# Optimization experiments

Hardware: AMD Instinct MI355X
Metric: run time of the kernel (lower is better)

The kernel has to match this reference:

```python
import jax, jax.numpy as jnp
import numpy as np

B, S, D = 2, 1024, 1024
H, HD = 16, 64
E_R = 31          # routed experts (n_experts - n_shared)
K_ACT = 3         # activated routed experts (n_activated - n_shared)
INTER = 1024      # expert inter dim = int(D*4*0.25)
EPS = 1e-5
BASE = 10000.0


def setup_inputs() -> dict:
    key = jax.random.key(0)
    ks = jax.random.split(key, 24)
    s = 0.02
    theta = (BASE ** (-jnp.arange(HD // 2, dtype=jnp.float32) * 2.0 / HD))
    inp = {
        'x': jax.random.normal(ks[0], (B, S, D), jnp.float32),
        'positions': jnp.arange(S, dtype=jnp.int32),
        'theta': theta,
        'gamma1': jnp.ones((D,), jnp.float32),
        'gamma2': jnp.ones((D,), jnp.float32),
        'q_w': jax.random.normal(ks[1], (D, H * HD), jnp.float32) * s,
        'q_b': jnp.zeros((H * HD,), jnp.float32),
        'k_w': jax.random.normal(ks[2], (D, H * HD), jnp.float32) * s,
        'k_b': jnp.zeros((H * HD,), jnp.float32),
        'v_w': jax.random.normal(ks[3], (D, H * HD), jnp.float32) * s,
        'v_b': jnp.zeros((H * HD,), jnp.float32),
        'o_w': jax.random.normal(ks[4], (H * HD, D), jnp.float32) * s,
        'o_b': jnp.zeros((D,), jnp.float32),
        'router_w': jax.random.normal(ks[5], (D, E_R), jnp.float32) * s,
        'router_b': jnp.zeros((E_R,), jnp.float32),
        'sh_w1': jax.random.normal(ks[6], (D, INTER), jnp.float32) * s,
        'sh_b1': jnp.zeros((INTER,), jnp.float32),
        'sh_w2': jax.random.normal(ks[7], (INTER, D), jnp.float32) * s,
        'sh_b2': jnp.zeros((D,), jnp.float32),
        're_w1': jax.random.normal(ks[8], (E_R, D, INTER), jnp.float32) * s,
        're_b1': jnp.zeros((E_R, INTER), jnp.float32),
        're_w2': jax.random.normal(ks[9], (E_R, INTER, D), jnp.float32) * s,
        're_b2': jnp.zeros((E_R, D), jnp.float32),
    }
    return inp


def _rmsnorm(x, gamma):
    rms = jnp.sqrt(jnp.mean(x * x, axis=-1, keepdims=True) + EPS)
    return x / rms * gamma


def _rope(x, theta):
    # x: [B,H,S,HD]; split even/odd, rotate, concat halves (matches source)
    seq = x.shape[2]
    angles = jnp.arange(seq, dtype=theta.dtype)[:, None] * theta  # [S, HD/2]
    cos = jnp.cos(angles)[None, None]
    sin = jnp.sin(angles)[None, None]
    x1, x2 = x[..., 0::2], x[..., 1::2]
    return jnp.concatenate([x1 * cos - x2 * sin, x1 * sin + x2 * cos], axis=-1)


def _forward(x, theta, gamma1, gamma2, q_w, q_b, k_w, k_b, v_w, v_b, o_w, o_b,
             router_w, router_b, sh_w1, sh_b1, sh_w2, sh_b2,
             re_w1, re_b1, re_w2, re_b2):
    b, s, d = x.shape
    xn = _rmsnorm(x, gamma1)
    # --- MHA ---
    q = (xn @ q_w + q_b).reshape(b, s, H, HD).transpose(0, 2, 1, 3)
    k = (xn @ k_w + k_b).reshape(b, s, H, HD).transpose(0, 2, 1, 3)
    v = (xn @ v_w + v_b).reshape(b, s, H, HD).transpose(0, 2, 1, 3)
    q = _rope(q, theta)
    k = _rope(k, theta)
    scale = 1.0 / np.sqrt(HD)
    scores = jnp.einsum('bhqd,bhkd->bhqk', q, k) * scale
    causal = jnp.tril(jnp.ones((s, s), dtype=bool))
    scores = jnp.where(causal, scores, -jnp.inf)
    attn = jax.nn.softmax(scores, axis=-1)
    ctx = jnp.einsum('bhqk,bhkd->bhqd', attn, v)
    ctx = ctx.transpose(0, 2, 1, 3).reshape(b, s, H * HD)
    attn_out = ctx @ o_w + o_b + xn
    # --- MoE ---
    an = _rmsnorm(attn_out, gamma2)
    shared = jax.nn.gelu(an @ sh_w1 + sh_b1, approximate=False) @ sh_w2 + sh_b2
    logits = an @ router_w + router_b                      # [B,S,E]
    aff = jax.nn.softmax(logits, axis=-1)
    topv, topi = jax.lax.top_k(aff, K_ACT)                 # [B,S,K]
    gates = jnp.sum(jax.nn.one_hot(topi, E_R, dtype=aff.dtype) * topv[..., None], axis=-2)  # [B,S,E]
    h = jax.nn.gelu(jnp.einsum('bsd,edh->besh', an, re_w1) + re_b1[None, :, None, :],
                    approximate=False)                     # [B,E,S,INTER]
    routed = jnp.einsum('bse,besh,ehd->bsd', gates, h, re_w2) \
           + jnp.einsum('bse,ed->bsd', gates, re_b2)
    return shared + routed + an + attn_out


def reference(x, positions, theta, gamma1, gamma2, q_w, q_b, k_w, k_b, v_w, v_b,
              o_w, o_b, router_w, router_b, sh_w1, sh_b1, sh_w2, sh_b2,
              re_w1, re_b1, re_w2, re_b2):
    del positions  # unused by the original forward (RoPE builds its own arange)
    return _forward(x, theta, gamma1, gamma2, q_w, q_b, k_w, k_b, v_w, v_b,
                    o_w, o_b, router_w, router_b, sh_w1, sh_b1, sh_w2, sh_b2,
                    re_w1, re_b1, re_w2, re_b2)
```

## Files before the change

kernel.cpp:

```cpp
#include <hip/hip_runtime.h>
#include <math.h>

typedef unsigned short u16;
typedef short s8v __attribute__((ext_vector_type(8)));
typedef u16 u4v __attribute__((ext_vector_type(4)));
typedef float f4v __attribute__((ext_vector_type(4)));

#define MFMA16(a,b,c) __builtin_amdgcn_mfma_f32_16x16x32_bf16((a),(b),(c),0,0,0)
#define GLDS16(g, l) __builtin_amdgcn_global_load_lds( \
    (const __attribute__((address_space(1))) unsigned int*)(g), \
    (__attribute__((address_space(3))) unsigned int*)(l), 16, 0, 0)

#define N_TOK 2048
#define SEQ   1024

__device__ __forceinline__ u16 f2b(float f){
  union { float f; unsigned u; } v; v.f = f;
  return (u16)((v.u + 0x7FFFu + ((v.u >> 16) & 1u)) >> 16);
}
__device__ __forceinline__ float b2f(u16 b){
  union { unsigned u; float f; } v; v.u = ((unsigned)b) << 16; return v.f;
}
__device__ __forceinline__ float gelu_f(float x){
  return 0.5f*x*(1.0f + erff(x*0.70710678118654752f));
}

__global__ __launch_bounds__(256) void rmsnorm_k(const float* __restrict__ x,
    const float* __restrict__ gamma, float* __restrict__ outf, u16* __restrict__ outb)
{
  const int t = blockIdx.x, tid = threadIdx.x;
  const float* xr = x + (size_t)t * 1024;
  float4 xv = *(const float4*)(xr + tid*4);
  float ss = xv.x*xv.x + xv.y*xv.y + xv.z*xv.z + xv.w*xv.w;
  #pragma unroll
  for (int off = 32; off; off >>= 1) ss += __shfl_down(ss, off);
  __shared__ float red[4];
  if ((tid & 63) == 0) red[tid >> 6] = ss;
  __syncthreads();
  float inv = rsqrtf((red[0]+red[1]+red[2]+red[3]) * (1.0f/1024.0f) + 1e-5f);
  float4 gv = *(const float4*)(gamma + tid*4);
  float4 o;
  o.x = xv.x*inv*gv.x; o.y = xv.y*inv*gv.y; o.z = xv.z*inv*gv.z; o.w = xv.w*inv*gv.w;
  *(float4*)(outf + (size_t)t*1024 + tid*4) = o;
  u4v ob = { f2b(o.x), f2b(o.y), f2b(o.z), f2b(o.w) };
  *(u4v*)(outb + (size_t)t*1024 + tid*4) = ob;
}

__device__ __forceinline__ void transT_body(const float* __restrict__ W, u16* __restrict__ Wt)
{
  __shared__ __align__(16) u16 T[64][68];
  const int tid = threadIdx.x;
  const int k0 = blockIdx.x*64, n0 = blockIdx.y*64;
  #pragma unroll
  for (int j = 0; j < 4; j++) {
    int q = j*256 + tid; int r = q >> 4, c4 = q & 15;
    float4 v = *(const float4*)(W + (size_t)(k0 + r)*1024 + n0 + c4*4);
    T[c4*4+0][r] = f2b(v.x); T[c4*4+1][r] = f2b(v.y);
    T[c4*4+2][r] = f2b(v.z); T[c4*4+3][r] = f2b(v.w);
  }
  __syncthreads();
  #pragma unroll
  for (int j = 0; j < 4; j++) {
    int q = j*256 + tid; int n = q >> 4, c4 = q & 15;
    u4v o = *(const u4v*)&T[n][c4*4];
    *(u4v*)(Wt + (size_t)(n0 + n)*1024 + k0 + c4*4) = o;
  }
}

__global__ __launch_bounds__(256) void transT6_k(
    const float* s0, const float* s1, const float* s2,
    const float* s3, const float* s4, const float* s5,
    u16* d0, u16* d1, u16* d2, u16* d3, u16* d4, u16* d5)
{
  const float* S; u16* D;
  switch (blockIdx.z) {
    case 0: S=s0; D=d0; break; case 1: S=s1; D=d1; break;
    case 2: S=s2; D=d2; break; case 3: S=s3; D=d3; break;
    case 4: S=s4; D=d4; break; default: S=s5; D=d5; break;
  }
  transT_body(S, D);
}

__global__ __launch_bounds__(256) void transv_k(const u16* __restrict__ vb, u16* __restrict__ vt)
{
  __shared__ __align__(16) u16 T[64][72];
  const int tid = threadIdx.x;
  const int s0 = blockIdx.x*64, bh = blockIdx.y, b = bh>>4, h = bh&15;
  #pragma unroll
  for (int j = 0; j < 16; j++) {
    int q = j*256 + tid; int r = q >> 6, c = q & 63;
    T[c][r] = vb[(size_t)(b*SEQ + s0 + r)*1024 + h*64 + c];
  }
  __syncthreads();
  #pragma unroll
  for (int i = 0; i < 2; i++) {
    int q = tid*2 + i; int rr = q >> 3, c8 = q & 7;
    *(s8v*)(vt + (size_t)(bh*64 + rr)*1024 + s0 + c8*8) = *(const s8v*)&T[rr][c8*8];
  }
}

template<int MODE, int BM, int BN>
__global__ __launch_bounds__(256) void mmk(
    const u16* __restrict__ A,
    const u16* __restrict__ Wt0, const u16* __restrict__ Wt1, const u16* __restrict__ Wt2,
    const float* __restrict__ bias0, const float* __restrict__ bias1, const float* __restrict__ bias2,
    float* __restrict__ outf, u16* __restrict__ outb0, u16* __restrict__ outb1, u16* __restrict__ outb2,
    const float* __restrict__ add1, const float* __restrict__ add2,
    const int* __restrict__ gidx, const float* __restrict__ gatel,
    const int* __restrict__ counts, const int* __restrict__ offs,
    const int* __restrict__ wl, const int* __restrict__ ntl,
    const float* __restrict__ theta, const float* __restrict__ wf)
{
  constexpr bool EW = (MODE == 5 || MODE == 6);
  constexpr int MF = BM/32, NF = BN/32;
  constexpr int CA = BM/32, CB = BN/32;
  constexpr int BST = EW ? 72 : 64;
  __shared__ __align__(16) u16 As[BM*64];
  __shared__ __align__(16) u16 Bs[BN*BST];
  __shared__ int toks[(MODE==5) ? BM : 1];
  __shared__ float gts[(MODE==6) ? BM : 1];

  const int tid = threadIdx.x;
  const int wave = tid >> 6, lane = tid & 63, quad = lane >> 4, l15 = lane & 15;
  int row0 = blockIdx.y * BM;
  int col0 = blockIdx.x * BN;
  const u16* Wt = Wt0;
  const float* bias = bias0;
  const u16* Ab = A;
  const float* Wf = wf;
  int wsel = 0, e = 0, cnt = 0, off_e = 0;

  if (MODE == 7) {
    wsel = blockIdx.x >> 3;
    col0 = (blockIdx.x & 7) * BN;
    Wt   = (wsel == 0) ? Wt0 : ((wsel == 1) ? Wt1 : Wt2);
    bias = (wsel == 0) ? bias0 : ((wsel == 1) ? bias1 : bias2);
  }
  if (EW) {
    if ((int)blockIdx.y >= ntl[0]) return;
    const int w = wl[blockIdx.y];
    e = w >> 8;
    row0 = (w & 255) * BM;
    cnt = counts[e];
    Wf = wf + (size_t)e * 1024 * 1024;
    bias = bias0 + e * 1024;
    off_e = offs[e];
    if (MODE == 6) Ab = A + (size_t)off_e * 1024;
    if (tid < BM) {
      int ok = (row0 + tid) < cnt;
      if (MODE == 5) toks[tid] = ok ? gidx[e * N_TOK + row0 + tid] : 0;
      if (MODE == 6) gts[tid]  = ok ? gatel[e * N_TOK + row0 + tid] : 0.f;
    }
    __syncthreads();
  }

  const int lr8 = lane >> 3;
  const int lk  = (lane & 7) * 8;
  const u16* aptr[CA];
  const u16* bptr[CB];
  #pragma unroll
  for (int c = 0; c < CA; c++) {
    const int ar = wave*(BM/4) + c*8 + lr8;
    long garow;
    if (MODE == 5) {
      garow = toks[ar];
    } else if (MODE == 6) {
      int rr = row0 + ar; if (rr >= cnt) rr = cnt - 1; garow = rr;
    } else {
      garow = row0 + ar;
    }
    aptr[c] = Ab + (size_t)garow * 1024 + lk;
  }
  if (!EW) {
    #pragma unroll
    for (int c = 0; c < CB; c++) {
      const int br = wave*(BN/4) + c*8 + lr8;
      bptr[c] = Wt + (size_t)(col0 + br) * 1024 + lk;
    }
  }

  const int ewn  = tid & 127;
  const int kg0  = (tid >> 7) * 4;
  const float* ewp = EW ? (Wf + (size_t)(kg0*8)*1024 + col0 + ewn) : nullptr;

  f4v acc[MF][NF];
  #pragma unroll
  for (int i = 0; i < MF; i++)
    #pragma unroll
    for (int j = 0; j < NF; j++)
      acc[i][j] = (f4v){0.f,0.f,0.f,0.f};

  const int wr = (wave >> 1) * (BM/2), wc = (wave & 1) * (BN/2);

  for (int k0 = 0; k0 < 1024; k0 += 64) {
    float fb[EW ? 4 : 1][EW ? 8 : 1];
    if (EW) {
      const float* wp = ewp + (size_t)k0 * 1024;
      #pragma unroll
      for (int it = 0; it < 4; it++)
        #pragma unroll
        for (int i = 0; i < 8; i++)
          fb[it][i] = wp[(size_t)(it*8 + i)*1024];
    }
    __syncthreads();
    #pragma unroll
    for (int c = 0; c < CA; c++) GLDS16(aptr[c] + k0, As + (wave*(BM/4) + c*8)*64);
    if (EW) {
      #pragma unroll
      for (int it = 0; it < 4; it++) {
        s8v h;
        #pragma unroll
        for (int i = 0; i < 8; i++) h[i] = (short)f2b(fb[it][i]);
        *(s8v*)&Bs[ewn*BST + (kg0 + it)*8] = h;
      }
    } else {
      #pragma unroll
      for (int c = 0; c < CB; c++) GLDS16(bptr[c] + k0, Bs + (wave*(BN/4) + c*8)*64);
    }
    __syncthreads();
    s8v af[2][MF], bfr[2][NF];
    #pragma unroll
    for (int ks = 0; ks < 2; ks++) {
      #pragma unroll
      for (int mt = 0; mt < MF; mt++) af[ks][mt]  = *(const s8v*)&As[(wr + mt*16 + l15)*64 + ks*32 + quad*8];
      #pragma unroll
      for (int nt = 0; nt < NF; nt++) bfr[ks][nt] = *(const s8v*)&Bs[(wc + nt*16 + l15)*BST + ks*32 + quad*8];
    }
    #pragma unroll
    for (int ks = 0; ks < 2; ks++)
      #pragma unroll
      for (int mt = 0; mt < MF; mt++)
        #pragma unroll
        for (int nt = 0; nt < NF; nt++)
          acc[mt][nt] = MFMA16(af[ks][mt], bfr[ks][nt], acc[mt][nt]);
  }

  #pragma unroll
  for (int mt = 0; mt < MF; mt++) {
    #pragma unroll
    for (int reg = 0; reg < 4; reg++) {
      const int lr = wr + mt*16 + quad*4 + reg;
      const size_t gr = row0 + lr;
      #pragma unroll
      for (int nt = 0; nt < NF; nt++) {
        const int n = wc + nt*16 + l15 + col0;
        float v = acc[mt][nt][reg] + bias[n];
        if (MODE == 7) {
          if (wsel == 2) {
            outb2[gr*1024 + n] = f2b(v);
          } else {
            float pv = __shfl_xor(v, 1);
            const int hd = n & 63;
            const int j = hd >> 1;
            const int s = (int)(gr & (SEQ - 1));
            float ang = (float)s * theta[j];
            float sn, cs;
            sincosf(ang, &sn, &cs);
            float res; int col;
            if (hd & 1) { res = pv*sn + v*cs; col = (n & ~63) | (32 + j); }
            else        { res = v*cs - pv*sn; col = (n & ~63) | j; }
            u16 bv = f2b(res);
            if (wsel == 0) outb0[gr*1024 + col] = bv;
            else           outb1[gr*1024 + col] = bv;
          }
        } else if (MODE == 3) {
          outf[gr*1024 + n] = v + add1[gr*1024 + n];
        } else if (MODE == 2) {
          outb0[gr*1024 + n] = f2b(gelu_f(v));
        } else if (MODE == 4) {
          outf[gr*1024 + n] = v + add1[gr*1024 + n] + add2[gr*1024 + n];
        } else if (MODE == 5) {
          if (row0 + lr < cnt)
            outb0[(size_t)(off_e + row0 + lr)*1024 + n] = f2b(gelu_f(v));
        } else if (MODE == 6) {
          if (row0 + lr < cnt)
            outf[(size_t)(off_e + row0 + lr)*1024 + n] = gts[lr] * v;
        }
      }
    }
  }
}

__global__ __launch_bounds__(256) void attn_k(const u16* __restrict__ qg,
    const u16* __restrict__ kg, const u16* __restrict__ vtg, u16* __restrict__ ctx)
{
  const int qt = (blockIdx.y < 16) ? blockIdx.x : (15 - blockIdx.x);
  const int bh = blockIdx.y, b = bh >> 4, h = bh & 15;
  const int tid = threadIdx.x, wave = tid >> 6, lane = tid & 63;
  const int quad = lane >> 4, l15 = lane & 15;
  __shared__ __align__(16) u16 Ks[64][72];
  __shared__ __align__(16) u16 Vt[64][72];
  __shared__ __align__(16) u16 Ps[4][16][72];

  s8v aq0, aq1;
  {
    const size_t qrow = (size_t)(b*SEQ + qt*64 + wave*16 + l15);
    aq0 = *(const s8v*)(qg + qrow*1024 + h*64 + quad*8);
    aq1 = *(const s8v*)(qg + qrow*1024 + h*64 + 32 + quad*8);
  }
  f4v oac[4];
  #pragma unroll
  for (int i = 0; i < 4; i++) oac[i] = (f4v){0.f,0.f,0.f,0.f};
  float mi[4] = {-INFINITY,-INFINITY,-INFINITY,-INFINITY};
  float li[4] = {0.f,0.f,0.f,0.f};

  for (int kt = 0; kt <= qt; kt++) {
    __syncthreads();
    #pragma unroll
    for (int ii = 0; ii < 2; ii++) {
      int c = tid*2 + ii, r = c >> 3, c8 = c & 7;
      *(s8v*)&Ks[r][c8*8] = *(const s8v*)(kg + (size_t)(b*SEQ + kt*64 + r)*1024 + h*64 + c8*8);
      *(s8v*)&Vt[r][c8*8] = *(const s8v*)(vtg + (size_t)(bh*64 + r)*1024 + kt*64 + c8*8);
    }
    __syncthreads();

    f4v s[4];
    #pragma unroll
    for (int nt = 0; nt < 4; nt++) {
      f4v z = (f4v){0.f,0.f,0.f,0.f};
      s8v bk0 = *(const s8v*)&Ks[nt*16 + l15][quad*8];
      s8v bk1 = *(const s8v*)&Ks[nt*16 + l15][32 + quad*8];
      z = MFMA16(aq0, bk0, z);
      z = MFMA16(aq1, bk1, z);
      s[nt] = z;
    }
    float sc[4][4];
    const int rowl = wave*16 + quad*4;
    #pragma unroll
    for (int nt = 0; nt < 4; nt++) {
      #pragma unroll
      for (int r = 0; r < 4; r++) {
        float v = s[nt][r] * 0.125f;
        if (kt == qt && (nt*16 + l15) > (rowl + r)) v = -INFINITY;
        sc[nt][r] = v;
      }
    }
    float alpha[4];
    #pragma unroll
    for (int r = 0; r < 4; r++) {
      float v0 = fmaxf(fmaxf(sc[0][r], sc[1][r]), fmaxf(sc[2][r], sc[3][r]));
      v0 = fmaxf(v0, __shfl_xor(v0, 1));
      v0 = fmaxf(v0, __shfl_xor(v0, 2));
      v0 = fmaxf(v0, __shfl_xor(v0, 4));
      v0 = fmaxf(v0, __shfl_xor(v0, 8));
      float mnew = fmaxf(mi[r], v0);
      alpha[r] = __expf(mi[r] - mnew);
      mi[r] = mnew;
    }
    float psum[4] = {0.f,0.f,0.f,0.f};
    #pragma unroll
    for (int nt = 0; nt < 4; nt++) {
      #pragma unroll
      for (int r = 0; r < 4; r++) {
        float p = __expf(sc[nt][r] - mi[r]);
        psum[r] += p;
        Ps[wave][quad*4 + r][nt*16 + l15] = f2b(p);
      }
    }
    #pragma unroll
    for (int r = 0; r < 4; r++) {
      float ps = psum[r];
      ps += __shfl_xor(ps, 1);
      ps += __shfl_xor(ps, 2);
      ps += __shfl_xor(ps, 4);
      ps += __shfl_xor(ps, 8);
      li[r] = li[r]*alpha[r] + ps;
    }
    #pragma unroll
    for (int ht = 0; ht < 4; ht++) {
      f4v o = oac[ht];
      o[0] *= alpha[0]; o[1] *= alpha[1]; o[2] *= alpha[2]; o[3] *= alpha[3];
      oac[ht] = o;
    }
    asm volatile("s_waitcnt lgkmcnt(0)" ::: "memory");
    s8v pf0 = *(const s8v*)&Ps[wave][l15][quad*8];
    s8v pf1 = *(const s8v*)&Ps[wave][l15][32 + quad*8];
    #pragma unroll
    for (int ht = 0; ht < 4; ht++) {
      s8v vf0 = *(const s8v*)&Vt[ht*16 + l15][quad*8];
      s8v vf1 = *(const s8v*)&Vt[ht*16 + l15][32 + quad*8];
      oac[ht] = MFMA16(pf0, vf0, oac[ht]);
      oac[ht] = MFMA16(pf1, vf1, oac[ht]);
    }
  }
  float inv[4];
  #pragma unroll
  for (int r = 0; r < 4; r++) inv[r] = 1.f / li[r];
  #pragma unroll
  for (int ht = 0; ht < 4; ht++) {
    #pragma unroll
    for (int r = 0; r < 4; r++) {
      size_t row = (size_t)(b*SEQ + qt*64 + wave*16 + quad*4 + r);
      ctx[row*1024 + h*64 + ht*16 + l15] = f2b(oac[ht][r] * inv[r]);
    }
  }
}

__global__ __launch_bounds__(256) void router_k(const float* __restrict__ an,
    const float* __restrict__ rw, const float* __restrict__ rb,
    int* __restrict__ counts, int* __restrict__ tok_list, float* __restrict__ gate_list,
    int* __restrict__ tok_e, int* __restrict__ tok_s)
{
  const int t = blockIdx.x, tid = threadIdx.x;
  const int e = tid & 31, ch = tid >> 5;
  float part = 0.f;
  if (e < 31) {
    const float* ar = an + (size_t)t*1024 + ch*128;
    const float* wp = rw + (size_t)(ch*128)*31 + e;
    #pragma unroll 8
    for (int d = 0; d < 128; d++) part += ar[d] * wp[d*31];
  }
  __shared__ float red[8][32];
  __shared__ float lgs[32];
  red[ch][e] = part;
  __syncthreads();
  if (tid < 31) {
    float s = 0.f;
    #pragma unroll
    for (int c = 0; c < 8; c++) s += red[c][tid];
    lgs[tid] = s + rb[tid];
  }
  __syncthreads();
  if (tid == 0) {
    float m = -1e30f;
    for (int i = 0; i < 31; i++) m = fmaxf(m, lgs[i]);
    float den = 0.f;
    for (int i = 0; i < 31; i++) den += __expf(lgs[i] - m);
    float invd = 1.f/den;
    unsigned used = 0;
    for (int kk = 0; kk < 3; kk++) {
      int best = 0; float bv = -3e30f;
      for (int i = 0; i < 31; i++) if (!((used>>i)&1u) && lgs[i] > bv) { bv = lgs[i]; best = i; }
      used |= (1u << best);
      float gate = __expf(lgs[best] - m) * invd;
      int slot = atomicAdd(&counts[best], 1);
      tok_list[best*N_TOK + slot] = t;
      gate_list[best*N_TOK + slot] = gate;
      tok_e[t*3 + kk] = best;
      tok_s[t*3 + kk] = slot;
    }
  }
}

__global__ void scan_k(const int* __restrict__ counts, int* __restrict__ offs,
                       int* __restrict__ wl, int* __restrict__ ntl){
  if (threadIdx.x == 0) {
    int s = 0, nt = 0;
    for (int i = 0; i < 31; i++){
      offs[i] = s; s += counts[i];
      int t = (counts[i] + 63) >> 6;
      for (int r = 0; r < t; r++) wl[nt++] = (i << 8) | r;
    }
    ntl[0] = nt;
  }
}

__global__ __launch_bounds__(256) void reduce_k(const float* __restrict__ mo,
    const int* __restrict__ tok_e, const int* __restrict__ tok_s,
    const int* __restrict__ offs, float* __restrict__ out)
{
  const int t = blockIdx.x, tid = threadIdx.x;
  float4 acc = *(const float4*)(out + (size_t)t*1024 + tid*4);
  #pragma unroll
  for (int j = 0; j < 3; j++) {
    int e = tok_e[t*3 + j], s = tok_s[t*3 + j];
    const float* row = mo + (size_t)(offs[e] + s) * 1024;
    float4 v = *(const float4*)(row + tid*4);
    acc.x += v.x; acc.y += v.y; acc.z += v.z; acc.w += v.w;
  }
  *(float4*)(out + (size_t)t*1024 + tid*4) = acc;
}

extern "C" void kernel_launch(void* const* d_in, const int* in_sizes, int n_in,
                              void* d_out, int out_size, void* d_ws, size_t ws_size,
                              hipStream_t stream)
{
  const float* x      = (const float*)d_in[0];
  const float* theta  = (const float*)d_in[2];
  const float* gamma1 = (const float*)d_in[3];
  const float* gamma2 = (const float*)d_in[4];
  const float* q_w = (const float*)d_in[5];
  const float* q_b = (const float*)d_in[6];
  const float* k_w = (const float*)d_in[7];
  const float* k_b = (const float*)d_in[8];
  const float* v_w = (const float*)d_in[9];
  const float* v_b = (const float*)d_in[10];
  const float* o_w = (const float*)d_in[11];
  const float* o_b = (const float*)d_in[12];
  const float* router_w = (const float*)d_in[13];
  const float* router_b = (const float*)d_in[14];
  const float* sh_w1 = (const float*)d_in[15];
  const float* sh_b1 = (const float*)d_in[16];
  const float* sh_w2 = (const float*)d_in[17];
  const float* sh_b2 = (const float*)d_in[18];
  const float* re_w1 = (const float*)d_in[19];
  const float* re_b1 = (const float*)d_in[20];
  const float* re_w2 = (const float*)d_in[21];
  const float* re_b2 = (const float*)d_in[22];
  float* out = (float*)d_out;

  char* p = (char*)d_ws;
  auto alloc = [&](size_t bytes) -> void* {
    void* r = (void*)p; p += (bytes + 255) & ~(size_t)255; return r;
  };
  const size_t F32 = (size_t)N_TOK*1024*4;
  const size_t B16 = (size_t)N_TOK*1024*2;
  float* xn       = (float*)alloc(F32);
  float* attn_out = (float*)alloc(F32);
  float* an       = (float*)alloc(F32);
  float* mo       = (float*)alloc((size_t)3*N_TOK*1024*4);
  u16* xnb  = (u16*)alloc(B16);
  u16* anb  = (u16*)alloc(B16);
  u16* vb   = (u16*)alloc(B16);
  u16* qb   = (u16*)alloc(B16);
  u16* kb   = (u16*)alloc(B16);
  u16* vt   = (u16*)alloc(B16);
  u16* ctxb = (u16*)alloc(B16);
  u16* shhb = (u16*)alloc(B16);
  u16* hmoe = (u16*)alloc((size_t)3*N_TOK*1024*2);
  u16* wtq  = (u16*)alloc((size_t)1024*1024*2);
  u16* wtk  = (u16*)alloc((size_t)1024*1024*2);
  u16* wtv  = (u16*)alloc((size_t)1024*1024*2);
  u16* wto  = (u16*)alloc((size_t)1024*1024*2);
  u16* wts1 = (u16*)alloc((size_t)1024*1024*2);
  u16* wts2 = (u16*)alloc((size_t)1024*1024*2);
  int* counts = (int*)alloc(128);
  int* offs   = (int*)alloc(128);
  int* tok_list  = (int*)alloc((size_t)31*N_TOK*4);
  float* gate_list = (float*)alloc((size_t)31*N_TOK*4);
  int* tok_e = (int*)alloc((size_t)N_TOK*3*4);
  int* tok_s = (int*)alloc((size_t)N_TOK*3*4);
  int* wl    = (int*)alloc(512);
  int* ntl   = (int*)alloc(64);

  hipMemsetAsync(counts, 0, 128, stream);

  transT6_k<<<dim3(16,16,6), 256, 0, stream>>>(q_w, k_w, v_w, o_w, sh_w1, sh_w2,
                                               wtq, wtk, wtv, wto, wts1, wts2);

  rmsnorm_k<<<N_TOK, 256, 0, stream>>>(x, gamma1, xn, xnb);

  mmk<7,64,128><<<dim3(24,32), 256, 0, stream>>>(xnb, wtq, wtk, wtv, q_b, k_b, v_b,
      nullptr, qb, kb, vb, nullptr, nullptr, nullptr, nullptr, nullptr, nullptr, nullptr, nullptr,
      theta, nullptr);

  transv_k<<<dim3(16,32), 256, 0, stream>>>(vb, vt);
  attn_k<<<dim3(16,32), 256, 0, stream>>>(qb, kb, vt, ctxb);

  mmk<3,64,64><<<dim3(16,32), 256, 0, stream>>>(ctxb, wto, nullptr, nullptr, o_b, nullptr, nullptr,
      attn_out, nullptr, nullptr, nullptr, xn, nullptr, nullptr, nullptr, nullptr, nullptr, nullptr, nullptr,
      nullptr, nullptr);

  rmsnorm_k<<<N_TOK, 256, 0, stream>>>(attn_out, gamma2, an, anb);

  mmk<2,64,64><<<dim3(16,32), 256, 0, stream>>>(anb, wts1, nullptr, nullptr, sh_b1, nullptr, nullptr,
      nullptr, shhb, nullptr, nullptr, nullptr, nullptr, nullptr, nullptr, nullptr, nullptr, nullptr, nullptr,
      nullptr, nullptr);

  router_k<<<N_TOK, 256, 0, stream>>>(an, router_w, router_b, counts, tok_list, gate_list, tok_e, tok_s);
  scan_k<<<1, 32, 0, stream>>>(counts, offs, wl, ntl);

  mmk<4,64,64><<<dim3(16,32), 256, 0, stream>>>(shhb, wts2, nullptr, nullptr, sh_b2, nullptr, nullptr,
      out, nullptr, nullptr, nullptr, an, attn_out, nullptr, nullptr, nullptr, nullptr, nullptr, nullptr,
      nullptr, nullptr);

  mmk<5,64,128><<<dim3(8,127), 256, 0, stream>>>(anb, nullptr, nullptr, nullptr, re_b1, nullptr, nullptr,
      nullptr, hmoe, nullptr, nullptr, nullptr, nullptr, tok_list, nullptr, counts, offs, wl, ntl,
      nullptr, re_w1);

  mmk<6,64,128><<<dim3(8,127), 256, 0, stream>>>(hmoe, nullptr, nullptr, nullptr, re_b2, nullptr, nullptr,
      mo, nullptr, nullptr, nullptr, nullptr, nullptr, tok_list, gate_list, counts, offs, wl, ntl,
      nullptr, re_w2);

  reduce_k<<<N_TOK, 256, 0, stream>>>(mo, tok_e, tok_s, offs, out);
}
```

Before: 604.8 us.

## Prefetch next expert-weight tile during MFMA and precompute RoPE sin/cos table

In the expert-weight GEMM modes, the next K-slice of the fp32 expert weights is now loaded into registers, and the next A tile into a second LDS buffer, while the current tile's MFMAs run. This hides global-load latency that was previously exposed before each iteration. Separately, a small kernel precomputes a per-position cos/sin table, so the QKV GEMM epilogue reads it instead of calling sincosf per element. The cost is more LDS for the A tiles, higher register pressure from the prefetch buffer, and one extra kernel launch.

```diff
diff --git a/kernel.cpp b/kernel.cpp
--- a/kernel.cpp
+++ b/kernel.cpp
@@ -46,6 +46,16 @@
   *(u4v*)(outb + (size_t)t*1024 + tid*4) = ob;
 }
 
+__global__ __launch_bounds__(256) void ropetab_k(const float* __restrict__ theta, float* __restrict__ tab)
+{
+  int i = blockIdx.x*256 + threadIdx.x;
+  int s = i >> 5, j = i & 31;
+  float sn, cs;
+  sincosf((float)s * theta[j], &sn, &cs);
+  tab[(size_t)s*64 + 2*j]     = cs;
+  tab[(size_t)s*64 + 2*j + 1] = sn;
+}
+
 __device__ __forceinline__ void transT_body(const float* __restrict__ W, u16* __restrict__ Wt)
 {
   __shared__ __align__(16) u16 T[64][68];
@@ -115,7 +125,7 @@
   constexpr int MF = BM/32, NF = BN/32;
   constexpr int CA = BM/32, CB = BN/32;
   constexpr int BST = EW ? 72 : 64;
-  __shared__ __align__(16) u16 As[BM*64];
+  __shared__ __align__(16) u16 As[(EW ? 2 : 1)*BM*64];
   __shared__ __align__(16) u16 Bs[BN*BST];
   __shared__ int toks[(MODE==5) ? BM : 1];
   __shared__ float gts[(MODE==6) ? BM : 1];
@@ -192,20 +202,19 @@
 
   const int wr = (wave >> 1) * (BM/2), wc = (wave & 1) * (BN/2);
 
-  for (int k0 = 0; k0 < 1024; k0 += 64) {
-    float fb[EW ? 4 : 1][EW ? 8 : 1];
-    if (EW) {
-      const float* wp = ewp + (size_t)k0 * 1024;
-      #pragma unroll
-      for (int it = 0; it < 4; it++)
-        #pragma unroll
-        for (int i = 0; i < 8; i++)
-          fb[it][i] = wp[(size_t)(it*8 + i)*1024];
-    }
-    __syncthreads();
-    #pragma unroll
-    for (int c = 0; c < CA; c++) GLDS16(aptr[c] + k0, As + (wave*(BM/4) + c*8)*64);
-    if (EW) {
+  if (EW) {
+    float fb[4][8];
+    #pragma unroll
+    for (int it = 0; it < 4; it++)
+      #pragma unroll
+      for (int i = 0; i < 8; i++)
+        fb[it][i] = ewp[(size_t)(it*8 + i)*1024];
+    #pragma unroll
+    for (int c = 0; c < CA; c++) GLDS16(aptr[c], As + (wave*(BM/4) + c*8)*64);
+
+    int buf = 0;
+    for (int k0 = 0; k0 < 1024; k0 += 64) {
+      __syncthreads();
       #pragma unroll
       for (int it = 0; it < 4; it++) {
         s8v h;
@@ -213,26 +222,59 @@
         for (int i = 0; i < 8; i++) h[i] = (short)f2b(fb[it][i]);
         *(s8v*)&Bs[ewn*BST + (kg0 + it)*8] = h;
       }
-    } else {
+      __syncthreads();
+      if (k0 + 64 < 1024) {
+        const float* wp = ewp + (size_t)(k0 + 64) * 1024;
+        #pragma unroll
+        for (int it = 0; it < 4; it++)
+          #pragma unroll
+          for (int i = 0; i < 8; i++)
+            fb[it][i] = wp[(size_t)(it*8 + i)*1024];
+        #pragma unroll
+        for (int c = 0; c < CA; c++)
+          GLDS16(aptr[c] + k0 + 64, As + ((buf^1)*BM + wave*(BM/4) + c*8)*64);
+      }
+      s8v af[2][MF], bfr[2][NF];
+      #pragma unroll
+      for (int ks = 0; ks < 2; ks++) {
+        #pragma unroll
+        for (int mt = 0; mt < MF; mt++) af[ks][mt]  = *(const s8v*)&As[(buf*BM + wr + mt*16 + l15)*64 + ks*32 + quad*8];
+        #pragma unroll
+        for (int nt = 0; nt < NF; nt++) bfr[ks][nt] = *(const s8v*)&Bs[(wc + nt*16 + l15)*BST + ks*32 + quad*8];
+      }
+      #pragma unroll
+      for (int ks = 0; ks < 2; ks++)
+        #pragma unroll
+        for (int mt = 0; mt < MF; mt++)
+          #pragma unroll
+          for (int nt = 0; nt < NF; nt++)
+            acc[mt][nt] = MFMA16(af[ks][mt], bfr[ks][nt], acc[mt][nt]);
+      buf ^= 1;
+    }
+  } else {
+    for (int k0 = 0; k0 < 1024; k0 += 64) {
+      __syncthreads();
+      #pragma unroll
+      for (int c = 0; c < CA; c++) GLDS16(aptr[c] + k0, As + (wave*(BM/4) + c*8)*64);
       #pragma unroll
       for (int c = 0; c < CB; c++) GLDS16(bptr[c] + k0, Bs + (wave*(BN/4) + c*8)*64);
-    }
-    __syncthreads();
-    s8v af[2][MF], bfr[2][NF];
-    #pragma unroll
-    for (int ks = 0; ks < 2; ks++) {
-      #pragma unroll
-      for (int mt = 0; mt < MF; mt++) af[ks][mt]  = *(const s8v*)&As[(wr + mt*16 + l15)*64 + ks*32 + quad*8];
-      #pragma unroll
-      for (int nt = 0; nt < NF; nt++) bfr[ks][nt] = *(const s8v*)&Bs[(wc + nt*16 + l15)*BST + ks*32 + quad*8];
-    }
-    #pragma unroll
-    for (int ks = 0; ks < 2; ks++)
-      #pragma unroll
-      for (int mt = 0; mt < MF; mt++)
-        #pragma unroll
-        for (int nt = 0; nt < NF; nt++)
-          acc[mt][nt] = MFMA16(af[ks][mt], bfr[ks][nt], acc[mt][nt]);
+      __syncthreads();
+      s8v af[2][MF], bfr[2][NF];
+      #pragma unroll
+      for (int ks = 0; ks < 2; ks++) {
+        #pragma unroll
+        for (int mt = 0; mt < MF; mt++) af[ks][mt]  = *(const s8v*)&As[(wr + mt*16 + l15)*64 + ks*32 + quad*8];
+        #pragma unroll
+        for (int nt = 0; nt < NF; nt++) bfr[ks][nt] = *(const s8v*)&Bs[(wc + nt*16 + l15)*BST + ks*32 + quad*8];
+      }
+      #pragma unroll
+      for (int ks = 0; ks < 2; ks++)
+        #pragma unroll
+        for (int mt = 0; mt < MF; mt++)
+          #pragma unroll
+          for (int nt = 0; nt < NF; nt++)
+            acc[mt][nt] = MFMA16(af[ks][mt], bfr[ks][nt], acc[mt][nt]);
+    }
   }
 
   #pragma unroll
@@ -253,9 +295,8 @@
             const int hd = n & 63;
             const int j = hd >> 1;
             const int s = (int)(gr & (SEQ - 1));
-            float ang = (float)s * theta[j];
-            float sn, cs;
-            sincosf(ang, &sn, &cs);
+            float2 t = *(const float2*)&theta[(size_t)s*64 + 2*j];
+            float cs = t.x, sn = t.y;
             float res; int col;
             if (hd & 1) { res = pv*sn + v*cs; col = (n & ~63) | (32 + j); }
             else        { res = v*cs - pv*sn; col = (n & ~63) | j; }
@@ -524,6 +565,7 @@
   u16* wto  = (u16*)alloc((size_t)1024*1024*2);
   u16* wts1 = (u16*)alloc((size_t)1024*1024*2);
   u16* wts2 = (u16*)alloc((size_t)1024*1024*2);
+  float* ropetab = (float*)alloc((size_t)SEQ*64*4);
   int* counts = (int*)alloc(128);
   int* offs   = (int*)alloc(128);
   int* tok_list  = (int*)alloc((size_t)31*N_TOK*4);
@@ -537,12 +579,13 @@
 
   transT6_k<<<dim3(16,16,6), 256, 0, stream>>>(q_w, k_w, v_w, o_w, sh_w1, sh_w2,
                                                wtq, wtk, wtv, wto, wts1, wts2);
+  ropetab_k<<<(SEQ*32)/256, 256, 0, stream>>>(theta, ropetab);
 
   rmsnorm_k<<<N_TOK, 256, 0, stream>>>(x, gamma1, xn, xnb);
 
   mmk<7,64,128><<<dim3(24,32), 256, 0, stream>>>(xnb, wtq, wtk, wtv, q_b, k_b, v_b,
       nullptr, qb, kb, vb, nullptr, nullptr, nullptr, nullptr, nullptr, nullptr, nullptr, nullptr,
-      theta, nullptr);
+      ropetab, nullptr);
 
   transv_k<<<dim3(16,32), 256, 0, stream>>>(vb, vt);
   attn_k<<<dim3(16,32), 256, 0, stream>>>(qb, kb, vt, ctxb);
```

After: 639.7 us. 1.06x slower.

## Enlarge MoE expert tiles, vectorize fp32 weight staging, precompute RoPE table

Applied to the files above, without the earlier changes.

The routed-expert GEMMs move from 64-row to 128-row tiles, so each expert's fp32 weights are read and converted to bf16 half as often. The scan and grid size are updated to match. The in-GEMM fp32 weight staging now uses float4 loads along N and transposes into LDS, where before it made scalar strided loads. RoPE sin/cos values come from a precomputed table built by a small extra kernel instead of per-element sincosf in the QKV epilogue. The risks are more padding waste for experts with few tokens, higher register pressure, and possible LDS bank conflicts on the transposed stores.

```diff
diff --git a/kernel.cpp b/kernel.cpp
--- a/kernel.cpp
+++ b/kernel.cpp
@@ -44,6 +44,16 @@
   *(float4*)(outf + (size_t)t*1024 + tid*4) = o;
   u4v ob = { f2b(o.x), f2b(o.y), f2b(o.z), f2b(o.w) };
   *(u4v*)(outb + (size_t)t*1024 + tid*4) = ob;
+}
+
+__global__ __launch_bounds__(256) void ropetab_k(const float* __restrict__ theta, float* __restrict__ tab)
+{
+  int i = blockIdx.x*256 + threadIdx.x;
+  int s = i >> 5, j = i & 31;
+  float sn, cs;
+  sincosf((float)s * theta[j], &sn, &cs);
+  tab[(size_t)s*64 + 2*j]     = cs;
+  tab[(size_t)s*64 + 2*j + 1] = sn;
 }
 
 __device__ __forceinline__ void transT_body(const float* __restrict__ W, u16* __restrict__ Wt)
@@ -179,9 +189,9 @@
     }
   }
 
-  const int ewn  = tid & 127;
-  const int kg0  = (tid >> 7) * 4;
-  const float* ewp = EW ? (Wf + (size_t)(kg0*8)*1024 + col0 + ewn) : nullptr;
+  const int ewnb = tid >> 3;
+  const int ewkb = tid & 7;
+  const float* ewp = EW ? (Wf + (size_t)(ewkb*8)*1024 + col0 + ewnb*4) : nullptr;
 
   f4v acc[MF][NF];
   #pragma unroll
@@ -193,25 +203,26 @@
   const int wr = (wave >> 1) * (BM/2), wc = (wave & 1) * (BN/2);
 
   for (int k0 = 0; k0 < 1024; k0 += 64) {
-    float fb[EW ? 4 : 1][EW ? 8 : 1];
+    float4 f[EW ? 8 : 1];
     if (EW) {
       const float* wp = ewp + (size_t)k0 * 1024;
       #pragma unroll
-      for (int it = 0; it < 4; it++)
-        #pragma unroll
-        for (int i = 0; i < 8; i++)
-          fb[it][i] = wp[(size_t)(it*8 + i)*1024];
+      for (int kk = 0; kk < 8; kk++)
+        f[kk] = *(const float4*)(wp + (size_t)kk * 1024);
     }
     __syncthreads();
     #pragma unroll
     for (int c = 0; c < CA; c++) GLDS16(aptr[c] + k0, As + (wave*(BM/4) + c*8)*64);
     if (EW) {
       #pragma unroll
-      for (int it = 0; it < 4; it++) {
+      for (int j = 0; j < 4; j++) {
         s8v h;
         #pragma unroll
-        for (int i = 0; i < 8; i++) h[i] = (short)f2b(fb[it][i]);
-        *(s8v*)&Bs[ewn*BST + (kg0 + it)*8] = h;
+        for (int kk = 0; kk < 8; kk++) {
+          float fv = (j == 0) ? f[kk].x : (j == 1) ? f[kk].y : (j == 2) ? f[kk].z : f[kk].w;
+          h[kk] = (short)f2b(fv);
+        }
+        *(s8v*)&Bs[(ewnb*4 + j)*BST + ewkb*8] = h;
       }
     } else {
       #pragma unroll
@@ -253,9 +264,8 @@
             const int hd = n & 63;
             const int j = hd >> 1;
             const int s = (int)(gr & (SEQ - 1));
-            float ang = (float)s * theta[j];
-            float sn, cs;
-            sincosf(ang, &sn, &cs);
+            float2 t = *(const float2*)&theta[(size_t)s*64 + 2*j];
+            float cs = t.x, sn = t.y;
             float res; int col;
             if (hd & 1) { res = pv*sn + v*cs; col = (n & ~63) | (32 + j); }
             else        { res = v*cs - pv*sn; col = (n & ~63) | j; }
@@ -448,7 +458,7 @@
     int s = 0, nt = 0;
     for (int i = 0; i < 31; i++){
       offs[i] = s; s += counts[i];
-      int t = (counts[i] + 63) >> 6;
+      int t = (counts[i] + 127) >> 7;
       for (int r = 0; r < t; r++) wl[nt++] = (i << 8) | r;
     }
     ntl[0] = nt;
@@ -524,6 +534,7 @@
   u16* wto  = (u16*)alloc((size_t)1024*1024*2);
   u16* wts1 = (u16*)alloc((size_t)1024*1024*2);
   u16* wts2 = (u16*)alloc((size_t)1024*1024*2);
+  float* ropetab = (float*)alloc((size_t)SEQ*64*4);
   int* counts = (int*)alloc(128);
   int* offs   = (int*)alloc(128);
   int* tok_list  = (int*)alloc((size_t)31*N_TOK*4);
@@ -537,12 +548,13 @@
 
   transT6_k<<<dim3(16,16,6), 256, 0, stream>>>(q_w, k_w, v_w, o_w, sh_w1, sh_w2,
                                                wtq, wtk, wtv, wto, wts1, wts2);
+  ropetab_k<<<(SEQ*32)/256, 256, 0, stream>>>(theta, ropetab);
 
   rmsnorm_k<<<N_TOK, 256, 0, stream>>>(x, gamma1, xn, xnb);
 
   mmk<7,64,128><<<dim3(24,32), 256, 0, stream>>>(xnb, wtq, wtk, wtv, q_b, k_b, v_b,
       nullptr, qb, kb, vb, nullptr, nullptr, nullptr, nullptr, nullptr, nullptr, nullptr, nullptr,
-      theta, nullptr);
+      ropetab, nullptr);
 
   transv_k<<<dim3(16,32), 256, 0, stream>>>(vb, vt);
   attn_k<<<dim3(16,32), 256, 0, stream>>>(qb, kb, vt, ctxb);
@@ -564,11 +576,11 @@
       out, nullptr, nullptr, nullptr, an, attn_out, nullptr, nullptr, nullptr, nullptr, nullptr, nullptr,
       nullptr, nullptr);
 
-  mmk<5,64,128><<<dim3(8,127), 256, 0, stream>>>(anb, nullptr, nullptr, nullptr, re_b1, nullptr, nullptr,
+  mmk<5,128,128><<<dim3(8,79), 256, 0, stream>>>(anb, nullptr, nullptr, nullptr, re_b1, nullptr, nullptr,
       nullptr, hmoe, nullptr, nullptr, nullptr, nullptr, tok_list, nullptr, counts, offs, wl, ntl,
       nullptr, re_w1);
 
-  mmk<6,64,128><<<dim3(8,127), 256, 0, stream>>>(hmoe, nullptr, nullptr, nullptr, re_b2, nullptr, nullptr,
+  mmk<6,128,128><<<dim3(8,79), 256, 0, stream>>>(hmoe, nullptr, nullptr, nullptr, re_b2, nullptr, nullptr,
       mo, nullptr, nullptr, nullptr, nullptr, nullptr, tok_list, gate_list, counts, offs, wl, ntl,
       nullptr, re_w2);
 
```

Result: faster. 564.4 us (-6.7%).
